# Performance work log

Measured on AMD Instinct MI355X. Metric: run time of the kernel, lower is better.

The kernel has to match this reference:

```python
import jax, jax.numpy as jnp
import numpy as np
from jax import lax

B, S, D, T = 64, 256, 1024, 60
HIST = 20  # last-20 window of attn / decoder-state history


def setup_inputs() -> dict:
    key = jax.random.key(0)
    ks = jax.random.split(key, 8)
    e_outputs = jax.random.normal(ks[0], (B, S, D), jnp.float32)
    queries = jax.random.normal(ks[1], (B, T, D), jnp.float32)
    # attention weights over source frames: rows sum to 1
    attns = jax.nn.softmax(jax.random.normal(ks[2], (B, T, S), jnp.float32), axis=-1)
    g = 0.02
    Wr = jax.random.normal(ks[3], (D, 1), jnp.float32) * g
    br = jnp.zeros((1,), jnp.float32)
    Wa = jax.random.normal(ks[4], (D, 1), jnp.float32) * g
    ba = jnp.zeros((1,), jnp.float32)
    Wq = jax.random.normal(ks[5], (D, D), jnp.float32) / np.sqrt(D)
    Wn = jax.random.normal(ks[6], (2 * D, 1), jnp.float32) * g
    bn = jnp.zeros((1,), jnp.float32)
    return {"e_outputs": e_outputs, "queries": queries, "attns": attns,
            "Wr": Wr, "br": br, "Wa": Wa, "ba": ba, "Wq": Wq, "Wn": Wn, "bn": bn}


def reference(e_outputs, queries, attns, Wr, br, Wa, ba, Wq, Wn, bn):
    Bn, Sn, Dn = e_outputs.shape
    # decay1[i] = (i+1)/20 ; decay2[i] = 1-(i+1)/50, zero-padded past 50 frames
    decay1 = (jnp.arange(HIST, dtype=jnp.float32) + 1.0) / 20.0
    idx = jnp.arange(Sn, dtype=jnp.float32)
    add0 = jnp.where(idx < 50, 1.0 - (idx + 1.0) / 50.0, 0.0)
    add_state0 = add0[None, :, None]                       # [1,S,1]
    mem0 = e_outputs * add_state0                          # [B,S,D]
    abuf0 = jnp.zeros((HIST, Bn, Sn), e_outputs.dtype)
    qbuf0 = jnp.zeros((HIST, Bn, Dn), e_outputs.dtype)

    def step(carry, x):
        mem, add_state, abuf, qbuf, i = carry
        attn_i, q_i = x                                    # [B,S], [B,D]
        # read: selected frame before memory update
        sel = jnp.einsum('bs,bsd->bd', attn_i, mem)
        # roll history buffers (newest at slot HIST-1)
        abuf = jnp.concatenate([abuf[1:], attn_i[None]], axis=0)
        qbuf = jnp.concatenate([qbuf[1:], q_i[None]], axis=0)
        k = jnp.minimum(i + 1, HIST)
        valid = jnp.arange(HIST) >= (HIST - k)
        temp = jax.nn.softmax(jnp.where(valid, decay1, -jnp.inf))
        attn_w = jnp.einsum('t,tbs->bs', temp, abuf)       # decayed attn sum
        query_s = jnp.einsum('t,tbd->bd', temp, qbuf)      # decayed query sum
        remove_prob = jax.nn.sigmoid(q_i @ Wr + br)[:, :, None]   # [B,1,1]
        add_prob = jax.nn.sigmoid(q_i @ Wa + ba)[:, :, None]      # [B,1,1]
        sim = jax.nn.sigmoid(jnp.einsum('bsd,bd->bs', mem, query_s @ Wq))[..., None]
        mem = mem * (1.0 - remove_prob * attn_w[..., None] * sim)
        last_ctx = jnp.einsum('bs,bsd->bd', attn_w, e_outputs)[:, None, :]
        cat = jnp.concatenate([e_outputs, jnp.broadcast_to(last_ctx, e_outputs.shape)], axis=-1)
        nxt = jax.nn.sigmoid(cat @ Wn + bn)                # [B,S,1]
        mem = mem + e_outputs * (1.0 - add_state) * (add_prob * nxt)
        add_state = add_state + (1.0 - add_state) * (add_prob * nxt)
        return (mem, add_state, abuf, qbuf, i + 1), sel

    init = (mem0, jnp.broadcast_to(add_state0, (Bn, Sn, 1)), abuf0, qbuf0, jnp.int32(0))
    xs = (attns.transpose(1, 0, 2), queries.transpose(1, 0, 2))
    _, sels = lax.scan(step, init, xs)
    return sels.transpose(1, 0, 2)                         # [B,T,D]
```

## Files before the change

### kernel.cpp

```cpp
#include <hip/hip_runtime.h>
#include <math.h>


#define Bn 64
#define Sn 256
#define Dn 1024
#define Tn 60
#define HISTn 20
#define LDK 72
#define K05 1.0512710963760241f
#define EINV 0.36787944117144233f

typedef __bf16 bf16x8 __attribute__((ext_vector_type(8)));
typedef float f32x4 __attribute__((ext_vector_type(4)));
typedef unsigned short us8 __attribute__((ext_vector_type(8)));

__device__ __forceinline__ unsigned short f2bf(float f){
  unsigned int x; __builtin_memcpy(&x,&f,4);
  unsigned int lsb = (x >> 16) & 1u;
  x += 0x7fffu + lsb;
  return (unsigned short)(x >> 16);
}
__device__ __forceinline__ float sigmoidf_(float x){ return 1.0f/(1.0f+expf(-x)); }

__global__ __launch_bounds__(256) void conv_qw(
    const float* __restrict__ Q, const float* __restrict__ Wr,
    const float* __restrict__ br, const float* __restrict__ Wa,
    const float* __restrict__ ba, const float* __restrict__ Wq,
    float* __restrict__ rp, float* __restrict__ ap,
    unsigned short* __restrict__ Qbf, unsigned short* __restrict__ WT)
{
  int tid = threadIdx.x;
  if (blockIdx.x < Bn*Tn){
    int row = blockIdx.x;
    float4 x = ((const float4*)(Q + (size_t)row*Dn))[tid];
    float4 a = ((const float4*)Wr)[tid];
    float4 b = ((const float4*)Wa)[tid];
    unsigned short o[4] = {f2bf(x.x), f2bf(x.y), f2bf(x.z), f2bf(x.w)};
    *(uint2*)&Qbf[(size_t)row*Dn + tid*4] = *(uint2*)o;
    float s1 = x.x*a.x + x.y*a.y + x.z*a.z + x.w*a.w;
    float s2 = x.x*b.x + x.y*b.y + x.z*b.z + x.w*b.w;
    for (int off = 32; off; off >>= 1){
      s1 += __shfl_down(s1, off, 64);
      s2 += __shfl_down(s2, off, 64);
    }
    __shared__ float r1[4], r2[4];
    int lane = tid & 63, wv = tid >> 6;
    if (lane == 0){ r1[wv] = s1; r2[wv] = s2; }
    __syncthreads();
    if (tid == 0){
      rp[row] = sigmoidf_(r1[0]+r1[1]+r1[2]+r1[3] + br[0]);
      ap[row] = sigmoidf_(r2[0]+r2[1]+r2[2]+r2[3] + ba[0]);
    }
  } else {
    __shared__ __align__(16) unsigned short Tt[64][LDK];
    int t = blockIdx.x - Bn*Tn;
    int n0 = (t >> 4)*64, k0 = (t & 15)*64;
    int kl = tid >> 4, nl4 = (tid & 15)*4;
    #pragma unroll
    for (int it = 0; it < 4; it++){
      int k = kl + it*16;
      float4 v = *(const float4*)&Wq[(size_t)(k0+k)*Dn + n0 + nl4];
      Tt[nl4+0][k] = f2bf(v.x); Tt[nl4+1][k] = f2bf(v.y);
      Tt[nl4+2][k] = f2bf(v.z); Tt[nl4+3][k] = f2bf(v.w);
    }
    __syncthreads();
    int nr = tid >> 2, kg = (tid & 3)*16;
    *(us8*)&WT[(size_t)(n0+nr)*Dn + k0+kg]   = *(us8*)&Tt[nr][kg];
    *(us8*)&WT[(size_t)(n0+nr)*Dn + k0+kg+8] = *(us8*)&Tt[nr][kg+8];
  }
}

__global__ __launch_bounds__(64) void conv_e(
    const float* __restrict__ E, const float* __restrict__ Wn,
    unsigned short* __restrict__ Ebf,
    float* __restrict__ eW1, float* __restrict__ eW2)
{
  int row = blockIdx.x, t = threadIdx.x;
  const float* er = E + (size_t)row*Dn;
  unsigned short* ebr = Ebf + (size_t)row*Dn;
  float d1 = 0.f, d2 = 0.f;
  #pragma unroll
  for (int c = 0; c < 4; c++){
    int idx = c*64 + t;
    float4 v = ((const float4*)er)[idx];
    float4 w1 = ((const float4*)Wn)[idx];
    float4 w2 = ((const float4*)(Wn + Dn))[idx];
    unsigned short o[4] = {f2bf(v.x), f2bf(v.y), f2bf(v.z), f2bf(v.w)};
    ((uint2*)ebr)[idx] = *(uint2*)o;
    d1 += v.x*w1.x + v.y*w1.y + v.z*w1.z + v.w*w1.w;
    d2 += v.x*w2.x + v.y*w2.y + v.z*w2.z + v.w*w2.w;
  }
  #pragma unroll
  for (int off = 32; off; off >>= 1){
    d1 += __shfl_down(d1, off, 64);
    d2 += __shfl_down(d2, off, 64);
  }
  if (t == 0){ eW1[row] = d1; eW2[row] = d2; }
}

__global__ __launch_bounds__(256) void gemm_qw(
    const unsigned short* __restrict__ Qbf,
    const unsigned short* __restrict__ WT,
    unsigned short* __restrict__ QWbf)
{
  __shared__ __align__(16) unsigned short As[64][LDK], Bs[64][LDK];
  int m0 = blockIdx.x*64, n0 = blockIdx.y*64;
  int tid = threadIdx.x, lane = tid & 63, wave = tid >> 6;
  int quad = lane >> 4, l16 = lane & 15;
  f32x4 acc[4];
  #pragma unroll
  for (int nt=0;nt<4;nt++)
    #pragma unroll
    for (int r=0;r<4;r++) acc[nt][r]=0.f;
  int sr = tid >> 2, sk = (tid & 3)*16;
  for (int k0 = 0; k0 < Dn; k0 += 64){
    *(us8*)&As[sr][sk]   = *(const us8*)&Qbf[(size_t)(m0+sr)*Dn + k0+sk];
    *(us8*)&As[sr][sk+8] = *(const us8*)&Qbf[(size_t)(m0+sr)*Dn + k0+sk+8];
    *(us8*)&Bs[sr][sk]   = *(const us8*)&WT[(size_t)(n0+sr)*Dn + k0+sk];
    *(us8*)&Bs[sr][sk+8] = *(const us8*)&WT[(size_t)(n0+sr)*Dn + k0+sk+8];
    __syncthreads();
    #pragma unroll
    for (int kk = 0; kk < 64; kk += 32){
      bf16x8 a = *(const bf16x8*)&As[wave*16 + l16][kk + quad*8];
      #pragma unroll
      for (int nt=0;nt<4;nt++){
        bf16x8 bb = *(const bf16x8*)&Bs[nt*16 + l16][kk + quad*8];
        acc[nt] = __builtin_amdgcn_mfma_f32_16x16x32_bf16(a, bb, acc[nt], 0, 0, 0);
      }
    }
    __syncthreads();
  }
  #pragma unroll
  for (int nt=0;nt<4;nt++)
    #pragma unroll
    for (int r=0;r<4;r++){
      int m = m0 + wave*16 + quad*4 + r;
      int n = n0 + nt*16 + l16;
      QWbf[(size_t)m*Dn + n] = f2bf(acc[nt][r]);
    }
}

__global__ __launch_bounds__(256) void gemm_g(
    const unsigned short* __restrict__ QWbf,
    const unsigned short* __restrict__ Ebf,
    float* __restrict__ G)
{
  __shared__ __align__(16) unsigned short As[64][LDK], Bs[32][LDK];
  int b = blockIdx.x, n0 = blockIdx.y*32;
  int tid = threadIdx.x, lane = tid & 63, wave = tid >> 6;
  int quad = lane >> 4, l16 = lane & 15;
  f32x4 acc[2];
  #pragma unroll
  for (int nt=0;nt<2;nt++)
    #pragma unroll
    for (int r=0;r<4;r++) acc[nt][r]=0.f;
  int sr = tid >> 2, sk = (tid & 3)*16;
  int brw = tid >> 3, bk = (tid & 7)*8;
  for (int k0 = 0; k0 < Dn; k0 += 64){
    if (sr < Tn){
      *(us8*)&As[sr][sk]   = *(const us8*)&QWbf[((size_t)(b*Tn + sr))*Dn + k0+sk];
      *(us8*)&As[sr][sk+8] = *(const us8*)&QWbf[((size_t)(b*Tn + sr))*Dn + k0+sk+8];
    } else {
      us8 z = (us8)0;
      *(us8*)&As[sr][sk] = z; *(us8*)&As[sr][sk+8] = z;
    }
    *(us8*)&Bs[brw][bk] = *(const us8*)&Ebf[((size_t)(b*Sn + n0 + brw))*Dn + k0 + bk];
    __syncthreads();
    #pragma unroll
    for (int kk = 0; kk < 64; kk += 32){
      bf16x8 a = *(const bf16x8*)&As[wave*16 + l16][kk + quad*8];
      #pragma unroll
      for (int nt=0;nt<2;nt++){
        bf16x8 bb = *(const bf16x8*)&Bs[nt*16 + l16][kk + quad*8];
        acc[nt] = __builtin_amdgcn_mfma_f32_16x16x32_bf16(a, bb, acc[nt], 0, 0, 0);
      }
    }
    __syncthreads();
  }
  #pragma unroll
  for (int nt=0;nt<2;nt++)
    #pragma unroll
    for (int r=0;r<4;r++){
      int t = wave*16 + quad*4 + r;
      int s = n0 + nt*16 + l16;
      if (t < Tn) G[((size_t)(b*Tn + t))*Sn + s] = acc[nt][r];
    }
}

__global__ __launch_bounds__(256) void kR_lc(
    const float* __restrict__ At,
    const float* __restrict__ eW2,
    float* __restrict__ lc)
{
  int b = blockIdx.x, tid = threadIdx.x;
  int lane = tid & 63, wv = tid >> 6;
  __shared__ float Rsh[Tn];
  float4 e2v = ((const float4*)(eW2 + (size_t)b*Sn))[lane];
  const float* at_b = At + (size_t)b*Tn*Sn;
  #pragma unroll
  for (int w = 0; w < 15; w++){
    int j = wv + w*4;
    float4 a4 = ((const float4*)(at_b + (size_t)j*Sn))[lane];
    float v = a4.x*e2v.x + a4.y*e2v.y + a4.z*e2v.z + a4.w*e2v.w;
    #pragma unroll
    for (int off = 32; off; off >>= 1) v += __shfl_down(v, off, 64);
    if (lane == 0) Rsh[j] = v;
  }
  __syncthreads();
  if (tid < Tn){
    int i = tid;
    int j0 = (i - HISTn + 1 > 0) ? i - HISTn + 1 : 0;
    float num = 0.f, den = 0.f;
    float wj = 1.f;
    for (int j = 0; j <= i; j++){
      wj *= K05;
      if (j >= j0){ num += wj * Rsh[j]; den += wj; }
    }
    lc[b*Tn + i] = num / den;
  }
}

__global__ __launch_bounds__(64) void scan_m(
    const float* __restrict__ At,
    const float* __restrict__ G,
    const float* __restrict__ rp,
    const float* __restrict__ ap,
    const float* __restrict__ eW1,
    const float* __restrict__ lc,
    const float* __restrict__ bnp,
    unsigned short* __restrict__ Pbf)
{
  int b = blockIdx.x, s0 = blockIdx.y * 64;
  int t = threadIdx.x;
  __shared__ __align__(16) float AtL[Tn][64], GL[Tn][64];
  __shared__ float lcs[Tn], rps[Tn], aps[Tn];
  const float* at_b = At + (size_t)b*Tn*Sn + s0;
  const float* g_b  = G  + (size_t)b*Tn*Sn + s0;
  #pragma unroll
  for (int r0 = 0; r0 < Tn; r0 += 4){
    int r = r0 + (t >> 4), c4 = (t & 15)*4;
    float4 av = *(const float4*)&at_b[(size_t)r*Sn + c4];
    float4 gv = *(const float4*)&g_b[(size_t)r*Sn + c4];
    *(float4*)&AtL[r][c4] = av;
    *(float4*)&GL[r][c4]  = gv;
  }
  if (t < Tn){
    lcs[t] = lc[b*Tn + t];
    rps[t] = rp[b*Tn + t];
    aps[t] = ap[b*Tn + t];
  }
  __syncthreads();
  int s = s0 + t;
  float M = (s < 50) ? (1.0f - (s+1)/50.0f) : 0.0f;
  float A = M;
  float bnv = bnp[0];
  float e1 = eW1[b*Sn + s];
  unsigned short* P_b = Pbf + (size_t)b*Tn*Sn + s;
  float num_a = 0.f, num_q = 0.f, den = 0.f, wi = 1.f;
  #pragma unroll
  for (int i = 0; i < Tn; i++){
    wi *= K05;
    float a_new = AtL[i][t];
    float g_new = GL[i][t];
    num_a += wi * a_new;
    num_q += wi * g_new;
    den   += wi;
    if (i >= HISTn){
      float wo = wi * EINV;
      num_a -= wo * AtL[i-HISTn][t];
      num_q -= wo * GL[i-HISTn][t];
      den   -= wo;
    }
    float inv = 1.0f / den;
    float aw = num_a * inv;
    float qd = num_q * inv;
    P_b[(size_t)i*Sn] = f2bf(a_new * M);
    float sim = sigmoidf_(M * qd);
    float nxt = sigmoidf_(e1 + lcs[i] + bnv);
    M = M * (1.0f - rps[i] * aw * sim);
    float g = (1.0f - A) * aps[i] * nxt;
    M += g; A += g;
  }
}

__global__ __launch_bounds__(256) void gemm_sels(
    const unsigned short* __restrict__ Pbf,
    const unsigned short* __restrict__ Ebf,
    float* __restrict__ out)
{
  __shared__ __align__(16) unsigned short As[64][LDK], Bs[64][LDK];
  int b = blockIdx.x, n0 = blockIdx.y*64;
  int tid = threadIdx.x, lane = tid & 63, wave = tid >> 6;
  int quad = lane >> 4, l16 = lane & 15;
  f32x4 acc[4];
  #pragma unroll
  for (int nt=0;nt<4;nt++)
    #pragma unroll
    for (int r=0;r<4;r++) acc[nt][r]=0.f;
  int sr = tid >> 2, sk = (tid & 3)*16;
  for (int k0 = 0; k0 < Sn; k0 += 64){
    if (sr < Tn){
      *(us8*)&As[sr][sk]   = *(const us8*)&Pbf[((size_t)(b*Tn + sr))*Sn + k0+sk];
      *(us8*)&As[sr][sk+8] = *(const us8*)&Pbf[((size_t)(b*Tn + sr))*Sn + k0+sk+8];
    } else {
      us8 z = (us8)0;
      *(us8*)&As[sr][sk] = z; *(us8*)&As[sr][sk+8] = z;
    }
    {
      const unsigned short* ep = &Ebf[((size_t)(b*Sn + k0 + sr))*Dn + n0 + sk];
      us8 e0 = *(const us8*)ep;
      us8 e1 = *(const us8*)(ep + 8);
      #pragma unroll
      for (int j=0;j<8;j++){
        Bs[sk+j][sr]   = e0[j];
        Bs[sk+8+j][sr] = e1[j];
      }
    }
    __syncthreads();
    #pragma unroll
    for (int kk = 0; kk < 64; kk += 32){
      bf16x8 a = *(const bf16x8*)&As[wave*16 + l16][kk + quad*8];
      #pragma unroll
      for (int nt=0;nt<4;nt++){
        bf16x8 bb = *(const bf16x8*)&Bs[nt*16 + l16][kk + quad*8];
        acc[nt] = __builtin_amdgcn_mfma_f32_16x16x32_bf16(a, bb, acc[nt], 0, 0, 0);
      }
    }
    __syncthreads();
  }
  #pragma unroll
  for (int nt=0;nt<4;nt++)
    #pragma unroll
    for (int r=0;r<4;r++){
      int t = wave*16 + quad*4 + r;
      int d = n0 + nt*16 + l16;
      if (t < Tn) out[((size_t)(b*Tn + t))*Dn + d] = acc[nt][r];
    }
}

extern "C" void kernel_launch(void* const* d_in, const int* in_sizes, int n_in,
                              void* d_out, int out_size, void* d_ws, size_t ws_size,
                              hipStream_t stream)
{
  const float* E  = (const float*)d_in[0];
  const float* Q  = (const float*)d_in[1];
  const float* At = (const float*)d_in[2];
  const float* Wr = (const float*)d_in[3];
  const float* br = (const float*)d_in[4];
  const float* Wa = (const float*)d_in[5];
  const float* ba = (const float*)d_in[6];
  const float* Wq = (const float*)d_in[7];
  const float* Wn = (const float*)d_in[8];
  const float* bnp= (const float*)d_in[9];

  char* ws = (char*)d_ws;
  float* rp  = (float*)ws; ws += (size_t)Bn*Tn*4;
  float* ap  = (float*)ws; ws += (size_t)Bn*Tn*4;
  float* eW1 = (float*)ws; ws += (size_t)Bn*Sn*4;
  float* eW2 = (float*)ws; ws += (size_t)Bn*Sn*4;
  float* lcb = (float*)ws; ws += (size_t)Bn*Tn*4;
  unsigned short* Qbf  = (unsigned short*)ws; ws += (size_t)Bn*Tn*Dn*2;
  unsigned short* WT   = (unsigned short*)ws; ws += (size_t)Dn*Dn*2;
  unsigned short* QWbf = (unsigned short*)ws; ws += (size_t)Bn*Tn*Dn*2;
  unsigned short* Ebf  = (unsigned short*)ws; ws += (size_t)Bn*Sn*Dn*2;
  float* G = (float*)ws; ws += (size_t)Bn*Tn*Sn*4;
  unsigned short* Pbf = (unsigned short*)ws; ws += (size_t)Bn*Tn*Sn*2;

  conv_qw<<<Bn*Tn + 256, 256, 0, stream>>>(Q, Wr, br, Wa, ba, Wq, rp, ap, Qbf, WT);
  conv_e<<<Bn*Sn, 64, 0, stream>>>(E, Wn, Ebf, eW1, eW2);
  gemm_qw<<<dim3(Bn*Tn/64, Dn/64), 256, 0, stream>>>(Qbf, WT, QWbf);
  gemm_g<<<dim3(Bn, Sn/32), 256, 0, stream>>>(QWbf, Ebf, G);
  kR_lc<<<Bn, 256, 0, stream>>>(At, eW2, lcb);
  scan_m<<<dim3(Bn, Sn/64), 64, 0, stream>>>(At, G, rp, ap, eW1, lcb, bnp, Pbf);
  gemm_sels<<<dim3(Bn, Dn/64), 256, 0, stream>>>(Pbf, Ebf, (float*)d_out);
}
```

Measured before the change: 210.0 us.

## Fuse encoder bf16 conversion and Wn dot products into consuming GEMMs

Removes the separate conv_e pass and its bf16 copy of the encoder outputs. gemm_g now loads fp32 E directly, converts it to bf16 in shared memory and computes the eW1/eW2 dot products with Wn along the way. gemm_sels also reads fp32 E and converts on the fly. This cuts one kernel launch and the write and re-read of an intermediate buffer. In exchange, both GEMMs read twice as many bytes for E and do extra conversion work per tile.

```diff
diff --git a/kernel.cpp b/kernel.cpp
--- a/kernel.cpp
+++ b/kernel.cpp
@@ -71,34 +71,6 @@
   }
 }
 
-__global__ __launch_bounds__(64) void conv_e(
-    const float* __restrict__ E, const float* __restrict__ Wn,
-    unsigned short* __restrict__ Ebf,
-    float* __restrict__ eW1, float* __restrict__ eW2)
-{
-  int row = blockIdx.x, t = threadIdx.x;
-  const float* er = E + (size_t)row*Dn;
-  unsigned short* ebr = Ebf + (size_t)row*Dn;
-  float d1 = 0.f, d2 = 0.f;
-  #pragma unroll
-  for (int c = 0; c < 4; c++){
-    int idx = c*64 + t;
-    float4 v = ((const float4*)er)[idx];
-    float4 w1 = ((const float4*)Wn)[idx];
-    float4 w2 = ((const float4*)(Wn + Dn))[idx];
-    unsigned short o[4] = {f2bf(v.x), f2bf(v.y), f2bf(v.z), f2bf(v.w)};
-    ((uint2*)ebr)[idx] = *(uint2*)o;
-    d1 += v.x*w1.x + v.y*w1.y + v.z*w1.z + v.w*w1.w;
-    d2 += v.x*w2.x + v.y*w2.y + v.z*w2.z + v.w*w2.w;
-  }
-  #pragma unroll
-  for (int off = 32; off; off >>= 1){
-    d1 += __shfl_down(d1, off, 64);
-    d2 += __shfl_down(d2, off, 64);
-  }
-  if (t == 0){ eW1[row] = d1; eW2[row] = d2; }
-}
-
 __global__ __launch_bounds__(256) void gemm_qw(
     const unsigned short* __restrict__ Qbf,
     const unsigned short* __restrict__ WT,
@@ -143,8 +115,9 @@
 
 __global__ __launch_bounds__(256) void gemm_g(
     const unsigned short* __restrict__ QWbf,
-    const unsigned short* __restrict__ Ebf,
-    float* __restrict__ G)
+    const float* __restrict__ E,
+    const float* __restrict__ Wn,
+    float* __restrict__ G, float* __restrict__ eW1, float* __restrict__ eW2)
 {
   __shared__ __align__(16) unsigned short As[64][LDK], Bs[32][LDK];
   int b = blockIdx.x, n0 = blockIdx.y*32;
@@ -157,6 +130,7 @@
     for (int r=0;r<4;r++) acc[nt][r]=0.f;
   int sr = tid >> 2, sk = (tid & 3)*16;
   int brw = tid >> 3, bk = (tid & 7)*8;
+  float d1 = 0.f, d2 = 0.f;
   for (int k0 = 0; k0 < Dn; k0 += 64){
     if (sr < Tn){
       *(us8*)&As[sr][sk]   = *(const us8*)&QWbf[((size_t)(b*Tn + sr))*Dn + k0+sk];
@@ -165,7 +139,20 @@
       us8 z = (us8)0;
       *(us8*)&As[sr][sk] = z; *(us8*)&As[sr][sk+8] = z;
     }
-    *(us8*)&Bs[brw][bk] = *(const us8*)&Ebf[((size_t)(b*Sn + n0 + brw))*Dn + k0 + bk];
+    const float* ep = &E[((size_t)(b*Sn + n0 + brw))*Dn + k0 + bk];
+    float4 e0 = *(const float4*)ep;
+    float4 e1 = *(const float4*)(ep + 4);
+    float4 w10 = *(const float4*)&Wn[k0 + bk];
+    float4 w11 = *(const float4*)&Wn[k0 + bk + 4];
+    float4 w20 = *(const float4*)&Wn[Dn + k0 + bk];
+    float4 w21 = *(const float4*)&Wn[Dn + k0 + bk + 4];
+    d1 += e0.x*w10.x + e0.y*w10.y + e0.z*w10.z + e0.w*w10.w
+        + e1.x*w11.x + e1.y*w11.y + e1.z*w11.z + e1.w*w11.w;
+    d2 += e0.x*w20.x + e0.y*w20.y + e0.z*w20.z + e0.w*w20.w
+        + e1.x*w21.x + e1.y*w21.y + e1.z*w21.z + e1.w*w21.w;
+    unsigned short cv[8] = {f2bf(e0.x), f2bf(e0.y), f2bf(e0.z), f2bf(e0.w),
+                            f2bf(e1.x), f2bf(e1.y), f2bf(e1.z), f2bf(e1.w)};
+    *(us8*)&Bs[brw][bk] = *(us8*)cv;
     __syncthreads();
     #pragma unroll
     for (int kk = 0; kk < 64; kk += 32){
@@ -177,6 +164,12 @@
       }
     }
     __syncthreads();
+  }
+  d1 += __shfl_down(d1, 4, 8); d1 += __shfl_down(d1, 2, 8); d1 += __shfl_down(d1, 1, 8);
+  d2 += __shfl_down(d2, 4, 8); d2 += __shfl_down(d2, 2, 8); d2 += __shfl_down(d2, 1, 8);
+  if ((tid & 7) == 0){
+    eW1[b*Sn + n0 + brw] = d1;
+    eW2[b*Sn + n0 + brw] = d2;
   }
   #pragma unroll
   for (int nt=0;nt<2;nt++)
@@ -286,7 +279,7 @@
 
 __global__ __launch_bounds__(256) void gemm_sels(
     const unsigned short* __restrict__ Pbf,
-    const unsigned short* __restrict__ Ebf,
+    const float* __restrict__ E,
     float* __restrict__ out)
 {
   __shared__ __align__(16) unsigned short As[64][LDK], Bs[64][LDK];
@@ -308,14 +301,15 @@
       *(us8*)&As[sr][sk] = z; *(us8*)&As[sr][sk+8] = z;
     }
     {
-      const unsigned short* ep = &Ebf[((size_t)(b*Sn + k0 + sr))*Dn + n0 + sk];
-      us8 e0 = *(const us8*)ep;
-      us8 e1 = *(const us8*)(ep + 8);
+      const float* ep = &E[((size_t)(b*Sn + k0 + sr))*Dn + n0 + sk];
+      float4 e0 = *(const float4*)ep;
+      float4 e1 = *(const float4*)(ep + 4);
+      float4 e2 = *(const float4*)(ep + 8);
+      float4 e3 = *(const float4*)(ep + 12);
+      float ev[16] = {e0.x,e0.y,e0.z,e0.w, e1.x,e1.y,e1.z,e1.w,
+                      e2.x,e2.y,e2.z,e2.w, e3.x,e3.y,e3.z,e3.w};
       #pragma unroll
-      for (int j=0;j<8;j++){
-        Bs[sk+j][sr]   = e0[j];
-        Bs[sk+8+j][sr] = e1[j];
-      }
+      for (int j=0;j<16;j++) Bs[sk+j][sr] = f2bf(ev[j]);
     }
     __syncthreads();
     #pragma unroll
@@ -363,15 +357,13 @@
   unsigned short* Qbf  = (unsigned short*)ws; ws += (size_t)Bn*Tn*Dn*2;
   unsigned short* WT   = (unsigned short*)ws; ws += (size_t)Dn*Dn*2;
   unsigned short* QWbf = (unsigned short*)ws; ws += (size_t)Bn*Tn*Dn*2;
-  unsigned short* Ebf  = (unsigned short*)ws; ws += (size_t)Bn*Sn*Dn*2;
   float* G = (float*)ws; ws += (size_t)Bn*Tn*Sn*4;
   unsigned short* Pbf = (unsigned short*)ws; ws += (size_t)Bn*Tn*Sn*2;
 
   conv_qw<<<Bn*Tn + 256, 256, 0, stream>>>(Q, Wr, br, Wa, ba, Wq, rp, ap, Qbf, WT);
-  conv_e<<<Bn*Sn, 64, 0, stream>>>(E, Wn, Ebf, eW1, eW2);
   gemm_qw<<<dim3(Bn*Tn/64, Dn/64), 256, 0, stream>>>(Qbf, WT, QWbf);
-  gemm_g<<<dim3(Bn, Sn/32), 256, 0, stream>>>(QWbf, Ebf, G);
+  gemm_g<<<dim3(Bn, Sn/32), 256, 0, stream>>>(QWbf, E, Wn, G, eW1, eW2);
   kR_lc<<<Bn, 256, 0, stream>>>(At, eW2, lcb);
   scan_m<<<dim3(Bn, Sn/64), 64, 0, stream>>>(At, G, rp, ap, eW1, lcb, bnp, Pbf);
-  gemm_sels<<<dim3(Bn, Dn/64), 256, 0, stream>>>(Pbf, Ebf, (float*)d_out);
-}
+  gemm_sels<<<dim3(Bn, Dn/64), 256, 0, stream>>>(Pbf, E, (float*)d_out);
+}
```

Measured after the change: 210.0 us. About the same (+0.0%).
